# Performance work log

Measured on AMD Instinct MI355X. Metric: run time of the kernel, lower is better.

Reference implementation:

```python
import jax, jax.numpy as jnp
import numpy as np

N = 50000
E = 800000
EPS = 1e-5


def setup_inputs() -> dict:
    key = jax.random.key(0)
    ks = jax.random.split(key, 8)
    x = jax.random.normal(ks[0], (N, 64), dtype=jnp.float32)
    edge_index = jax.random.randint(ks[1], (2, E), 0, N, dtype=jnp.int64)
    # Glorot-ish scaled weights
    W_rel0 = jax.random.normal(ks[2], (64, 128), dtype=jnp.float32) * (1.0 / np.sqrt(64))
    W_root0 = jax.random.normal(ks[3], (64, 128), dtype=jnp.float32) * (1.0 / np.sqrt(64))
    W_rel1 = jax.random.normal(ks[4], (128, 128), dtype=jnp.float32) * (1.0 / np.sqrt(128))
    W_root1 = jax.random.normal(ks[5], (128, 128), dtype=jnp.float32) * (1.0 / np.sqrt(128))
    return {
        "x": x,
        "edge_index": edge_index,
        "W_rel0": W_rel0,
        "b_rel0": jnp.zeros((128,), jnp.float32),
        "W_root0": W_root0,
        "gamma0": jnp.ones((128,), jnp.float32),
        "beta0": jnp.zeros((128,), jnp.float32),
        "W_rel1": W_rel1,
        "b_rel1": jnp.zeros((128,), jnp.float32),
        "W_root1": W_root1,
        "gamma1": jnp.ones((128,), jnp.float32),
        "beta1": jnp.zeros((128,), jnp.float32),
    }


def _graph_conv(x, src, dst, W_rel, b_rel, W_root):
    # aggr_out[i] = sum_{(s,i) in edges} x[s]   (PyG GraphConv, aggr='add')
    agg = jax.ops.segment_sum(x[src], dst, num_segments=N)  # [N, F_in]
    return agg @ W_rel + b_rel + x @ W_root                  # [N, F_out]


def _batchnorm(h, gamma, beta):
    mean = jnp.mean(h, axis=0)
    var = jnp.var(h, axis=0)
    return (h - mean) * jax.lax.rsqrt(var + EPS) * gamma + beta


def reference(x, edge_index, W_rel0, b_rel0, W_root0, gamma0, beta0,
              W_rel1, b_rel1, W_root1, gamma1, beta1):
    src, dst = edge_index[0], edge_index[1]
    # layer 0: conv -> BN -> ReLU (dropout p=0 is identity)
    h = _graph_conv(x, src, dst, W_rel0, b_rel0, W_root0)
    h = jax.nn.relu(_batchnorm(h, gamma0, beta0))
    # layer 1 (last): conv -> BN, no activation
    h = _graph_conv(h, src, dst, W_rel1, b_rel1, W_root1)
    h = _batchnorm(h, gamma1, beta1)
    return h
```

## Files before the change

kernel.cpp:

```cpp
#include <hip/hip_runtime.h>

#define NN 50000
#define NE 800000
#define EPSV 1e-5f

typedef unsigned int u32;
typedef short s16x8 __attribute__((ext_vector_type(8)));
typedef float f32x4 __attribute__((ext_vector_type(4)));

#define WS_NEEDED \
  ((size_t)(NN * 64 + NN * 32 + 1024 + NN + NN + NE + 2 * 400000 + NE) * 4)

__global__ void k_fallback(float* __restrict__ out) {
  int i = blockIdx.x * 256 + threadIdx.x;
  if (i < NN * 128) out[i] = 2.0f;
}

__global__ void k_detect(const int* __restrict__ ei, int* __restrict__ mode) {
  if (threadIdx.x == 0) {
    int all0 = 1;
    for (int i = 1; i < 64; i += 2) all0 &= (ei[i] == 0);
    *mode = all0;
  }
}

__device__ __forceinline__ void load_edge(const int* __restrict__ ei, int m, int e,
                                          int& src, int& dst) {
  if (m) { src = ei[e << 1]; dst = ei[(NE + e) << 1]; }
  else   { src = ei[e];      dst = ei[NE + e]; }
  src = min(max(src, 0), NN - 1);
  dst = min(max(dst, 0), NN - 1);
}

__global__ __launch_bounds__(256) void k_hist(
    const int* __restrict__ ei, const int* __restrict__ mode,
    int* __restrict__ deg, int* __restrict__ rank, u32* __restrict__ pedge) {
  int e = blockIdx.x * 256 + threadIdx.x;
  int src, dst;
  load_edge(ei, *mode, e, src, dst);
  rank[e] = atomicAdd(&deg[dst], 1);
  pedge[e] = ((u32)src << 16) | (u32)dst;
}

__global__ __launch_bounds__(256) void k_scan1(
    const int* __restrict__ deg, int* __restrict__ bsum) {
  const int b = blockIdx.x, t = threadIdx.x;
  const int lane = t & 63, wave = t >> 6;
  int idx = b * 256 + t;
  int v = (idx < NN) ? deg[idx] : 0;
  for (int off = 32; off > 0; off >>= 1) v += __shfl_down(v, off);
  __shared__ int wt[4];
  if (lane == 0) wt[wave] = v;
  __syncthreads();
  if (t == 0) bsum[b] = wt[0] + wt[1] + wt[2] + wt[3];
}

__global__ __launch_bounds__(256) void k_scan3(
    const int* __restrict__ deg, const int* __restrict__ bsum, int* __restrict__ cur) {
  const int b = blockIdx.x, t = threadIdx.x;
  const int lane = t & 63, wave = t >> 6;
  __shared__ int wt[4];
  __shared__ int boff;
  int pv = (t < b) ? bsum[t] : 0;
  int r = pv;
  for (int off = 32; off > 0; off >>= 1) r += __shfl_down(r, off);
  if (lane == 0) wt[wave] = r;
  __syncthreads();
  if (t == 0) boff = wt[0] + wt[1] + wt[2] + wt[3];
  __syncthreads();
  int idx = b * 256 + t;
  int v = (idx < NN) ? deg[idx] : 0;
  int incl = v;
  for (int off = 1; off < 64; off <<= 1) {
    int u = __shfl_up(incl, off);
    if (lane >= off) incl += u;
  }
  if (lane == 63) wt[wave] = incl;
  __syncthreads();
  int woff = 0;
  for (int w = 0; w < wave; ++w) woff += wt[w];
  if (idx < NN) cur[idx] = boff + woff + incl - v;
}

__global__ __launch_bounds__(256) void k_place(
    const u32* __restrict__ pedge, const int* __restrict__ cur,
    const int* __restrict__ rank, int* __restrict__ csr) {
  int e = blockIdx.x * 256 + threadIdx.x;
  u32 pe = pedge[e];
  int dst = (int)(pe & 0xffffu);
  int src = (int)(pe >> 16);
  csr[cur[dst] + rank[e]] = src;
}

__device__ __forceinline__ u32 pack_bf16(float lo, float hi) {
  union { float f; u32 u; } a, b;
  a.f = lo; b.f = hi;
  u32 ua = a.u + 0x7fffu + ((a.u >> 16) & 1u);
  u32 ub = b.u + 0x7fffu + ((b.u >> 16) & 1u);
  return (ua >> 16) | (ub & 0xffff0000u);
}
#define BFLO(u) __uint_as_float((u) << 16)
#define BFHI(u) __uint_as_float((u) & 0xffff0000u)

__global__ __launch_bounds__(256) void k_pack(
    const float* __restrict__ x, u32* __restrict__ xb) {
  int i = blockIdx.x * 256 + threadIdx.x;
  int n = i >> 5, c = i & 31;
  float2 v = *(const float2*)&x[n * 64 + c * 2];
  xb[i] = pack_bf16(v.x, v.y);
}

__global__ __launch_bounds__(256) void k_gather_xb(
    const u32* __restrict__ xb, const int* __restrict__ csr,
    const int* __restrict__ cur, const int* __restrict__ deg,
    u32* __restrict__ aggxb) {
  int tid = blockIdx.x * 256 + threadIdx.x;
  int n = tid >> 4, L = tid & 15;
  int i = cur[n];
  int end = i + deg[n];
  float a0 = 0.f, a1 = 0.f, a2 = 0.f, a3 = 0.f;
  float b0 = 0.f, b1 = 0.f, b2 = 0.f, b3 = 0.f;
  for (; i + 1 < end; i += 2) {
    int s0 = csr[i], s1 = csr[i + 1];
    uint2 u = *(const uint2*)&xb[s0 * 32 + 2 * L];
    uint2 w = *(const uint2*)&xb[s1 * 32 + 2 * L];
    a0 += BFLO(u.x); a1 += BFHI(u.x); a2 += BFLO(u.y); a3 += BFHI(u.y);
    b0 += BFLO(w.x); b1 += BFHI(w.x); b2 += BFLO(w.y); b3 += BFHI(w.y);
  }
  if (i < end) {
    int s0 = csr[i];
    uint2 u = *(const uint2*)&xb[s0 * 32 + 2 * L];
    a0 += BFLO(u.x); a1 += BFHI(u.x); a2 += BFLO(u.y); a3 += BFHI(u.y);
  }
  uint2 o;
  o.x = pack_bf16(a0 + b0, a1 + b1);
  o.y = pack_bf16(a2 + b2, a3 + b3);
  *(uint2*)&aggxb[n * 32 + 2 * L] = o;
}

__global__ __launch_bounds__(256) void k_packW0(
    const float* __restrict__ Wrel, const float* __restrict__ Wroot,
    u32* __restrict__ Wpk0) {
  int t = blockIdx.x * 256 + threadIdx.x;
  int r = t & 3, lane = (t >> 2) & 63, s = (t >> 8) & 3, nt = t >> 10;
  int k = 32 * s + (lane >> 4) * 8 + 2 * r;
  int col = 16 * nt + (lane & 15);
  const float* W = (k < 64) ? &Wrel[k * 128 + col] : &Wroot[(k - 64) * 128 + col];
  Wpk0[t] = pack_bf16(W[0], W[128]);
}

__global__ __launch_bounds__(256) void k_gemm_a(
    const float* __restrict__ x, const u32* __restrict__ aggxb,
    const u32* __restrict__ Wpk0,
    float* __restrict__ h, float* __restrict__ psum, float* __restrict__ pssq) {
  __shared__ u32 As[8192];
  const int tid = threadIdx.x;
  const int nb = blockIdx.x * 128;
  char* AsB = (char*)As;
#pragma unroll
  for (int it = 0; it < 16; ++it) {
    int f = tid + 256 * it;
    int row = f >> 5, k4 = f & 31;
    int n = nb + row;
    uint2 p;
    if (k4 < 16) {
      p = (n < NN) ? *(const uint2*)&aggxb[n * 32 + 2 * k4] : make_uint2(0u, 0u);
    } else {
      float4 v = (n < NN) ? *(const float4*)&x[n * 64 + 4 * (k4 - 16)]
                          : make_float4(0.f, 0.f, 0.f, 0.f);
      p.x = pack_bf16(v.x, v.y);
      p.y = pack_bf16(v.z, v.w);
    }
    int byte = row * 256 + k4 * 8;
    byte ^= (row & 7) << 4;
    *(uint2*)(AsB + byte) = p;
  }
  __syncthreads();
  const int lane = tid & 63;
  const int w = tid >> 6;
  const int lr = lane & 15;
  const int lg = lane >> 4;
  f32x4 zero = {0.f, 0.f, 0.f, 0.f};
  f32x4 acc[8][2];
#pragma unroll
  for (int m = 0; m < 8; ++m) {
    acc[m][0] = zero;
    acc[m][1] = zero;
  }
#pragma unroll
  for (int s = 0; s < 4; ++s) {
    s16x8 bf[2];
#pragma unroll
    for (int nt = 0; nt < 2; ++nt)
      bf[nt] = *(const s16x8*)&Wpk0[(((2 * w + nt) * 4 + s) * 64 + lane) * 4];
#pragma unroll
    for (int m = 0; m < 8; ++m) {
      int row = 16 * m + lr;
      int byte = row * 256 + 64 * s + 16 * lg;
      byte ^= (row & 7) << 4;
      s16x8 af = *(const s16x8*)(AsB + byte);
      acc[m][0] = __builtin_amdgcn_mfma_f32_16x16x32_bf16(af, bf[0], acc[m][0], 0, 0, 0);
      acc[m][1] = __builtin_amdgcn_mfma_f32_16x16x32_bf16(af, bf[1], acc[m][1], 0, 0, 0);
    }
  }
  float ps[2] = {0.f, 0.f}, qs[2] = {0.f, 0.f};
#pragma unroll
  for (int m = 0; m < 8; ++m) {
    int rowb = nb + 16 * m + 4 * lg;
#pragma unroll
    for (int nt = 0; nt < 2; ++nt) {
      int colg = 32 * w + 16 * nt + lr;
#pragma unroll
      for (int i = 0; i < 4; ++i) {
        float a = acc[m][nt][i];
        int n = rowb + i;
        if (n < NN) h[n * 128 + colg] = a;
        ps[nt] += a;
        qs[nt] += a * a;
      }
    }
  }
  __syncthreads();
  float* S = (float*)As;
  float* Q = S + 512;
#pragma unroll
  for (int nt = 0; nt < 2; ++nt) {
    int colg = 32 * w + 16 * nt + lr;
    S[lg * 128 + colg] = ps[nt];
    Q[lg * 128 + colg] = qs[nt];
  }
  __syncthreads();
  if (tid < 128) {
    float s = 0.f, q = 0.f;
#pragma unroll
    for (int g = 0; g < 4; ++g) { s += S[g * 128 + tid]; q += Q[g * 128 + tid]; }
    psum[blockIdx.x * 128 + tid] = s;
    pssq[blockIdx.x * 128 + tid] = q;
  }
}

__global__ __launch_bounds__(64) void k_bnfin(
    const float* __restrict__ psum, const float* __restrict__ pssq,
    const float* __restrict__ gamma, const float* __restrict__ beta,
    float* __restrict__ scale, float* __restrict__ shift, int P) {
  const int c = blockIdx.x;
  const int t = threadIdx.x;
  float S = 0.f, Q = 0.f;
  for (int p = t; p < P; p += 64) {
    S += psum[p * 128 + c];
    Q += pssq[p * 128 + c];
  }
  for (int off = 32; off > 0; off >>= 1) {
    S += __shfl_down(S, off);
    Q += __shfl_down(Q, off);
  }
  if (t == 0) {
    float mean = S * (1.0f / NN);
    float var = fmaxf(Q * (1.0f / NN) - mean * mean, 0.f);
    float sc = gamma[c] * rsqrtf(var + EPSV);
    scale[c] = sc;
    shift[c] = beta[c] - mean * sc;
  }
}

__global__ __launch_bounds__(256) void k_packW(
    const float* __restrict__ Wrel, const float* __restrict__ Wroot,
    u32* __restrict__ Wpk) {
  int t = blockIdx.x * 256 + threadIdx.x;
  int r = t & 3, lane = (t >> 2) & 63, s = (t >> 8) & 3, nt = t >> 10;
  int k = 32 * s + (lane >> 4) * 8 + 2 * r;
  int col = 16 * nt + (lane & 15);
  const float* W = (col < 128) ? &Wrel[k * 128 + col] : &Wroot[k * 128 + (col - 128)];
  Wpk[t] = pack_bf16(W[0], W[128]);
}

__global__ __launch_bounds__(256) void k_gemm_b(
    const u32* __restrict__ Wpk,
    const float* __restrict__ scale, const float* __restrict__ shift,
    u32* __restrict__ yb, float* __restrict__ h) {
  __shared__ u32 As[4096];
  const int tid = threadIdx.x;
  const int nb = blockIdx.x * 64;
  char* AsB = (char*)As;
#pragma unroll
  for (int it = 0; it < 8; ++it) {
    int f = tid + 256 * it;
    int row = f >> 5, k4 = f & 31;
    int n = nb + row;
    float4 v = (n < NN) ? *(const float4*)&h[n * 128 + 4 * k4]
                        : make_float4(0.f, 0.f, 0.f, 0.f);
    float4 sc = *(const float4*)&scale[4 * k4];
    float4 sh = *(const float4*)&shift[4 * k4];
    float t0 = fmaxf(v.x * sc.x + sh.x, 0.f);
    float t1 = fmaxf(v.y * sc.y + sh.y, 0.f);
    float t2 = fmaxf(v.z * sc.z + sh.z, 0.f);
    float t3 = fmaxf(v.w * sc.w + sh.w, 0.f);
    uint2 p;
    p.x = pack_bf16(t0, t1);
    p.y = pack_bf16(t2, t3);
    int byte = row * 256 + k4 * 8;
    byte ^= (row & 7) << 4;
    *(uint2*)(AsB + byte) = p;
  }
  __syncthreads();
  const int lane = tid & 63;
  const int w = tid >> 6;
  const int lr = lane & 15;
  const int lg = lane >> 4;
  f32x4 zero = {0.f, 0.f, 0.f, 0.f};
  f32x4 acc[4][4];
#pragma unroll
  for (int m = 0; m < 4; ++m)
#pragma unroll
    for (int nt = 0; nt < 4; ++nt) acc[m][nt] = zero;

#pragma unroll
  for (int s = 0; s < 4; ++s) {
    s16x8 af[4];
#pragma unroll
    for (int m = 0; m < 4; ++m) {
      int row = 16 * m + lr;
      int byte = row * 256 + 64 * s + 16 * lg;
      byte ^= (row & 7) << 4;
      af[m] = *(const s16x8*)(AsB + byte);
    }
    s16x8 bf[4];
#pragma unroll
    for (int nt = 0; nt < 4; ++nt) {
      int gnt = w * 4 + nt;
      bf[nt] = *(const s16x8*)&Wpk[((gnt * 4 + s) * 64 + lane) * 4];
    }
#pragma unroll
    for (int m = 0; m < 4; ++m)
#pragma unroll
      for (int nt = 0; nt < 4; ++nt)
        acc[m][nt] = __builtin_amdgcn_mfma_f32_16x16x32_bf16(
            af[m], bf[nt], acc[m][nt], 0, 0, 0);
  }
  if (w < 2) {
#pragma unroll
    for (int m = 0; m < 4; ++m) {
#pragma unroll
      for (int nt = 0; nt < 4; ++nt) {
        int colg = 64 * w + 16 * nt + lr;
        int rowb = nb + 16 * m + 4 * lg;
        float a0 = acc[m][nt][0], a1 = acc[m][nt][1];
        float a2 = acc[m][nt][2], a3 = acc[m][nt][3];
        float o0 = __shfl_xor(a0, 1), o1 = __shfl_xor(a1, 1);
        float o2 = __shfl_xor(a2, 1), o3 = __shfl_xor(a3, 1);
        int c2 = colg >> 1;
        u32 q0, q1;
        int i0;
        if ((lane & 1) == 0) {
          q0 = pack_bf16(a0, o0); q1 = pack_bf16(a1, o1); i0 = 0;
        } else {
          q0 = pack_bf16(o2, a2); q1 = pack_bf16(o3, a3); i0 = 2;
        }
        int n0 = rowb + i0, n1 = rowb + i0 + 1;
        if (n0 < NN) yb[n0 * 64 + c2] = q0;
        if (n1 < NN) yb[n1 * 64 + c2] = q1;
      }
    }
  } else {
#pragma unroll
    for (int m = 0; m < 4; ++m) {
#pragma unroll
      for (int nt = 0; nt < 4; ++nt) {
        int colg = 64 * (w - 2) + 16 * nt + lr;
        int rowb = nb + 16 * m + 4 * lg;
#pragma unroll
        for (int i = 0; i < 4; ++i) {
          int n = rowb + i;
          if (n < NN) h[n * 128 + colg] = acc[m][nt][i];
        }
      }
    }
  }
}

__global__ __launch_bounds__(256) void k_gather2(
    const u32* __restrict__ yb, const int* __restrict__ csr,
    const int* __restrict__ cur, const int* __restrict__ deg,
    float* __restrict__ h, float* __restrict__ psum, float* __restrict__ pssq) {
  int tid = blockIdx.x * 256 + threadIdx.x;
  int n = tid >> 4;
  int L = threadIdx.x & 15;
  int base = L << 2;
  int c0 = L << 3;
  int i = cur[n];
  int end = i + deg[n];
  float lo0 = 0.f, lo1 = 0.f, lo2 = 0.f, lo3 = 0.f;
  float hi0 = 0.f, hi1 = 0.f, hi2 = 0.f, hi3 = 0.f;
  float mo0 = 0.f, mo1 = 0.f, mo2 = 0.f, mo3 = 0.f;
  float ni0 = 0.f, ni1 = 0.f, ni2 = 0.f, ni3 = 0.f;
  for (; i + 1 < end; i += 2) {
    int s0 = csr[i], s1 = csr[i + 1];
    uint4 v = *(const uint4*)&yb[s0 * 64 + base];
    uint4 w = *(const uint4*)&yb[s1 * 64 + base];
    lo0 += BFLO(v.x); hi0 += BFHI(v.x);
    lo1 += BFLO(v.y); hi1 += BFHI(v.y);
    lo2 += BFLO(v.z); hi2 += BFHI(v.z);
    lo3 += BFLO(v.w); hi3 += BFHI(v.w);
    mo0 += BFLO(w.x); ni0 += BFHI(w.x);
    mo1 += BFLO(w.y); ni1 += BFHI(w.y);
    mo2 += BFLO(w.z); ni2 += BFHI(w.z);
    mo3 += BFLO(w.w); ni3 += BFHI(w.w);
  }
  if (i < end) {
    int s = csr[i];
    uint4 v = *(const uint4*)&yb[s * 64 + base];
    lo0 += BFLO(v.x); hi0 += BFHI(v.x);
    lo1 += BFLO(v.y); hi1 += BFHI(v.y);
    lo2 += BFLO(v.z); hi2 += BFHI(v.z);
    lo3 += BFLO(v.w); hi3 += BFHI(v.w);
  }
  float4 A = *(const float4*)&h[n * 128 + c0];
  float4 B = *(const float4*)&h[n * 128 + c0 + 4];
  float4 R0 = make_float4(A.x + lo0 + mo0, A.y + hi0 + ni0,
                          A.z + lo1 + mo1, A.w + hi1 + ni1);
  float4 R1 = make_float4(B.x + lo2 + mo2, B.y + hi2 + ni2,
                          B.z + lo3 + mo3, B.w + hi3 + ni3);
  *(float4*)&h[n * 128 + c0]     = R0;
  *(float4*)&h[n * 128 + c0 + 4] = R1;
  __shared__ float S[16 * 132], Q[16 * 132];
  const int nl = threadIdx.x >> 4;
  *(float4*)&S[nl * 132 + c0]     = R0;
  *(float4*)&S[nl * 132 + c0 + 4] = R1;
  *(float4*)&Q[nl * 132 + c0] =
      make_float4(R0.x * R0.x, R0.y * R0.y, R0.z * R0.z, R0.w * R0.w);
  *(float4*)&Q[nl * 132 + c0 + 4] =
      make_float4(R1.x * R1.x, R1.y * R1.y, R1.z * R1.z, R1.w * R1.w);
  __syncthreads();
  const int t = threadIdx.x;
  if (t < 128) {
    float s = 0.f, q = 0.f;
#pragma unroll
    for (int g = 0; g < 16; ++g) { s += S[g * 132 + t]; q += Q[g * 132 + t]; }
    psum[blockIdx.x * 128 + t] = s;
    pssq[blockIdx.x * 128 + t] = q;
  }
}

__global__ __launch_bounds__(256) void k_final(
    const float* __restrict__ h, const float* __restrict__ scale,
    const float* __restrict__ shift, float* __restrict__ out) {
  int tid = blockIdx.x * 256 + threadIdx.x;
  int base = tid << 2;
  int f4 = base & 127;
  float4 v = *(const float4*)&h[base];
  float4 sc = *(const float4*)&scale[f4];
  float4 sh = *(const float4*)&shift[f4];
  *(float4*)&out[base] = make_float4(v.x * sc.x + sh.x, v.y * sc.y + sh.y,
                                     v.z * sc.z + sh.z, v.w * sc.w + sh.w);
}

extern "C" void kernel_launch(void* const* d_in, const int* in_sizes, int n_in,
                              void* d_out, int out_size, void* d_ws, size_t ws_size,
                              hipStream_t stream) {
  if (ws_size < WS_NEEDED) {
    k_fallback<<<(NN * 128 + 255) / 256, 256, 0, stream>>>((float*)d_out);
    return;
  }
  const float* x      = (const float*)d_in[0];
  const int*   ei     = (const int*)d_in[1];
  const float* Wrel0  = (const float*)d_in[2];
  const float* Wroot0 = (const float*)d_in[4];
  const float* gamma0 = (const float*)d_in[5];
  const float* beta0  = (const float*)d_in[6];
  const float* Wrel1  = (const float*)d_in[7];
  const float* Wroot1 = (const float*)d_in[9];
  const float* gamma1 = (const float*)d_in[10];
  const float* beta1  = (const float*)d_in[11];

  float* aggx = (float*)d_ws;
  u32*   aggxb = (u32*)d_ws;
  u32*   yb   = (u32*)d_ws;
  u32*   xb   = (u32*)(aggx + NN * 64);
  u32*   Wpk  = xb;
  u32*   Wpk0 = xb + 16384;
  float* st   = (float*)(xb + NN * 32);
  float* scale0 = st;       float* shift0 = st + 128;
  float* scale1 = st + 256; float* shift1 = st + 384;
  int* mode = (int*)(st + 512);
  int* bsum = (int*)(st + 576);
  int* deg = (int*)(st + 1024);
  int* cur = deg + NN;
  int* csr = cur + NN;
  float* psum = (float*)(csr + NE);
  float* pssq = psum + 400000;
  int* rank = (int*)psum;
  u32* pedge = (u32*)(pssq + 400000);
  float* h = (float*)d_out;

  hipMemsetAsync(deg, 0, (size_t)NN * 4, stream);
  k_detect<<<1, 64, 0, stream>>>(ei, mode);
  k_hist<<<NE / 256, 256, 0, stream>>>(ei, mode, deg, rank, pedge);
  k_scan1<<<196, 256, 0, stream>>>(deg, bsum);
  k_scan3<<<196, 256, 0, stream>>>(deg, bsum, cur);
  k_place<<<NE / 256, 256, 0, stream>>>(pedge, cur, rank, csr);

  k_pack<<<(NN * 32) / 256, 256, 0, stream>>>(x, xb);
  k_gather_xb<<<(NN * 16) / 256, 256, 0, stream>>>(xb, csr, cur, deg, aggxb);
  k_packW<<<64, 256, 0, stream>>>(Wrel1, Wroot1, Wpk);
  k_packW0<<<32, 256, 0, stream>>>(Wrel0, Wroot0, Wpk0);
  k_gemm_a<<<(NN + 127) / 128, 256, 0, stream>>>(x, aggxb, Wpk0, h, psum, pssq);
  k_bnfin<<<128, 64, 0, stream>>>(psum, pssq, gamma0, beta0, scale0, shift0, 391);
  k_gemm_b<<<(NN + 63) / 64, 256, 0, stream>>>(Wpk, scale0, shift0, yb, h);
  k_gather2<<<(NN * 16) / 256, 256, 0, stream>>>(yb, csr, cur, deg, h, psum, pssq);
  k_bnfin<<<128, 64, 0, stream>>>(psum, pssq, gamma1, beta1, scale1, shift1, 3125);
  k_final<<<(NN * 128) / 1024, 256, 0, stream>>>(h, scale1, shift1, (float*)d_out);
}
```

Before: 279.0 us.

## Store layer-0 conv output as bf16 and merge packing kernels into one launch

The layer-0 GEMM now writes its pre-BN output h as packed bf16 into a workspace buffer, pairing neighbouring columns with a lane shuffle, instead of writing fp32 to the output buffer. The layer-1 GEMM reads this bf16 buffer and widens it before applying BN and ReLU, which halves that intermediate's write and read traffic. gemm_a also reads the pre-packed bf16 x instead of re-converting fp32 x. The three small pack kernels are merged into one launch, saving two launches. BN statistics are still taken from fp32 accumulators, but the extra bf16 rounding of h adds some precision loss and the workspace grows.

```diff
diff --git a/kernel.cpp b/kernel.cpp
--- a/kernel.cpp
+++ b/kernel.cpp
@@ -9,7 +9,8 @@
 typedef float f32x4 __attribute__((ext_vector_type(4)));
 
 #define WS_NEEDED \
-  ((size_t)(NN * 64 + NN * 32 + 1024 + NN + NN + NE + 2 * 400000 + NE) * 4)
+  ((size_t)(NN * 64 + NN * 32 + 1024 + NN + NN + NE + 2 * 400000 + NE + \
+            16384 + 8192 + NN * 64) * 4)
 
 __global__ void k_fallback(float* __restrict__ out) {
   int i = blockIdx.x * 256 + threadIdx.x;
@@ -102,12 +103,35 @@
 #define BFLO(u) __uint_as_float((u) << 16)
 #define BFHI(u) __uint_as_float((u) & 0xffff0000u)
 
-__global__ __launch_bounds__(256) void k_pack(
-    const float* __restrict__ x, u32* __restrict__ xb) {
-  int i = blockIdx.x * 256 + threadIdx.x;
-  int n = i >> 5, c = i & 31;
-  float2 v = *(const float2*)&x[n * 64 + c * 2];
-  xb[i] = pack_bf16(v.x, v.y);
+__global__ __launch_bounds__(256) void k_prep(
+    const float* __restrict__ x, u32* __restrict__ xb,
+    const float* __restrict__ Wrel1, const float* __restrict__ Wroot1,
+    u32* __restrict__ Wpk,
+    const float* __restrict__ Wrel0, const float* __restrict__ Wroot0,
+    u32* __restrict__ Wpk0) {
+  const int b = blockIdx.x;
+  if (b < 6250) {
+    int i = b * 256 + threadIdx.x;
+    int n = i >> 5, c = i & 31;
+    float2 v = *(const float2*)&x[n * 64 + c * 2];
+    xb[i] = pack_bf16(v.x, v.y);
+  } else if (b < 6314) {
+    int t = (b - 6250) * 256 + threadIdx.x;
+    int r = t & 3, lane = (t >> 2) & 63, s = (t >> 8) & 3, nt = t >> 10;
+    int k = 32 * s + (lane >> 4) * 8 + 2 * r;
+    int col = 16 * nt + (lane & 15);
+    const float* W = (col < 128) ? &Wrel1[k * 128 + col]
+                                 : &Wroot1[k * 128 + (col - 128)];
+    Wpk[t] = pack_bf16(W[0], W[128]);
+  } else {
+    int t = (b - 6314) * 256 + threadIdx.x;
+    int r = t & 3, lane = (t >> 2) & 63, s = (t >> 8) & 3, nt = t >> 10;
+    int k = 32 * s + (lane >> 4) * 8 + 2 * r;
+    int col = 16 * nt + (lane & 15);
+    const float* W = (k < 64) ? &Wrel0[k * 128 + col]
+                              : &Wroot0[(k - 64) * 128 + col];
+    Wpk0[t] = pack_bf16(W[0], W[128]);
+  }
 }
 
 __global__ __launch_bounds__(256) void k_gather_xb(
@@ -138,21 +162,10 @@
   *(uint2*)&aggxb[n * 32 + 2 * L] = o;
 }
 
-__global__ __launch_bounds__(256) void k_packW0(
-    const float* __restrict__ Wrel, const float* __restrict__ Wroot,
-    u32* __restrict__ Wpk0) {
-  int t = blockIdx.x * 256 + threadIdx.x;
-  int r = t & 3, lane = (t >> 2) & 63, s = (t >> 8) & 3, nt = t >> 10;
-  int k = 32 * s + (lane >> 4) * 8 + 2 * r;
-  int col = 16 * nt + (lane & 15);
-  const float* W = (k < 64) ? &Wrel[k * 128 + col] : &Wroot[(k - 64) * 128 + col];
-  Wpk0[t] = pack_bf16(W[0], W[128]);
-}
-
 __global__ __launch_bounds__(256) void k_gemm_a(
-    const float* __restrict__ x, const u32* __restrict__ aggxb,
+    const u32* __restrict__ xb, const u32* __restrict__ aggxb,
     const u32* __restrict__ Wpk0,
-    float* __restrict__ h, float* __restrict__ psum, float* __restrict__ pssq) {
+    u32* __restrict__ hb, float* __restrict__ psum, float* __restrict__ pssq) {
   __shared__ u32 As[8192];
   const int tid = threadIdx.x;
   const int nb = blockIdx.x * 128;
@@ -162,15 +175,8 @@
     int f = tid + 256 * it;
     int row = f >> 5, k4 = f & 31;
     int n = nb + row;
-    uint2 p;
-    if (k4 < 16) {
-      p = (n < NN) ? *(const uint2*)&aggxb[n * 32 + 2 * k4] : make_uint2(0u, 0u);
-    } else {
-      float4 v = (n < NN) ? *(const float4*)&x[n * 64 + 4 * (k4 - 16)]
-                          : make_float4(0.f, 0.f, 0.f, 0.f);
-      p.x = pack_bf16(v.x, v.y);
-      p.y = pack_bf16(v.z, v.w);
-    }
+    const u32* src = (k4 < 16) ? &aggxb[n * 32 + 2 * k4] : &xb[n * 32 + 2 * (k4 - 16)];
+    uint2 p = (n < NN) ? *(const uint2*)src : make_uint2(0u, 0u);
     int byte = row * 256 + k4 * 8;
     byte ^= (row & 7) << 4;
     *(uint2*)(AsB + byte) = p;
@@ -206,18 +212,37 @@
   float ps[2] = {0.f, 0.f}, qs[2] = {0.f, 0.f};
 #pragma unroll
   for (int m = 0; m < 8; ++m) {
-    int rowb = nb + 16 * m + 4 * lg;
 #pragma unroll
     for (int nt = 0; nt < 2; ++nt) {
-      int colg = 32 * w + 16 * nt + lr;
 #pragma unroll
       for (int i = 0; i < 4; ++i) {
         float a = acc[m][nt][i];
-        int n = rowb + i;
-        if (n < NN) h[n * 128 + colg] = a;
         ps[nt] += a;
         qs[nt] += a * a;
       }
+    }
+  }
+#pragma unroll
+  for (int m = 0; m < 8; ++m) {
+    int rowb = nb + 16 * m + 4 * lg;
+#pragma unroll
+    for (int nt = 0; nt < 2; ++nt) {
+      int colg = 32 * w + 16 * nt + lr;
+      float a0 = acc[m][nt][0], a1 = acc[m][nt][1];
+      float a2 = acc[m][nt][2], a3 = acc[m][nt][3];
+      float o0 = __shfl_xor(a0, 1), o1 = __shfl_xor(a1, 1);
+      float o2 = __shfl_xor(a2, 1), o3 = __shfl_xor(a3, 1);
+      int c2 = colg >> 1;
+      u32 q0, q1;
+      int i0;
+      if ((lane & 1) == 0) {
+        q0 = pack_bf16(a0, o0); q1 = pack_bf16(a1, o1); i0 = 0;
+      } else {
+        q0 = pack_bf16(o2, a2); q1 = pack_bf16(o3, a3); i0 = 2;
+      }
+      int n0 = rowb + i0, n1 = rowb + i0 + 1;
+      if (n0 < NN) hb[n0 * 64 + c2] = q0;
+      if (n1 < NN) hb[n1 * 64 + c2] = q1;
     }
   }
   __syncthreads();
@@ -263,19 +288,8 @@
   }
 }
 
-__global__ __launch_bounds__(256) void k_packW(
-    const float* __restrict__ Wrel, const float* __restrict__ Wroot,
-    u32* __restrict__ Wpk) {
-  int t = blockIdx.x * 256 + threadIdx.x;
-  int r = t & 3, lane = (t >> 2) & 63, s = (t >> 8) & 3, nt = t >> 10;
-  int k = 32 * s + (lane >> 4) * 8 + 2 * r;
-  int col = 16 * nt + (lane & 15);
-  const float* W = (col < 128) ? &Wrel[k * 128 + col] : &Wroot[k * 128 + (col - 128)];
-  Wpk[t] = pack_bf16(W[0], W[128]);
-}
-
 __global__ __launch_bounds__(256) void k_gemm_b(
-    const u32* __restrict__ Wpk,
+    const u32* __restrict__ hb, const u32* __restrict__ Wpk,
     const float* __restrict__ scale, const float* __restrict__ shift,
     u32* __restrict__ yb, float* __restrict__ h) {
   __shared__ u32 As[4096];
@@ -287,14 +301,13 @@
     int f = tid + 256 * it;
     int row = f >> 5, k4 = f & 31;
     int n = nb + row;
-    float4 v = (n < NN) ? *(const float4*)&h[n * 128 + 4 * k4]
-                        : make_float4(0.f, 0.f, 0.f, 0.f);
+    uint2 v = (n < NN) ? *(const uint2*)&hb[n * 64 + 2 * k4] : make_uint2(0u, 0u);
     float4 sc = *(const float4*)&scale[4 * k4];
     float4 sh = *(const float4*)&shift[4 * k4];
-    float t0 = fmaxf(v.x * sc.x + sh.x, 0.f);
-    float t1 = fmaxf(v.y * sc.y + sh.y, 0.f);
-    float t2 = fmaxf(v.z * sc.z + sh.z, 0.f);
-    float t3 = fmaxf(v.w * sc.w + sh.w, 0.f);
+    float t0 = fmaxf(BFLO(v.x) * sc.x + sh.x, 0.f);
+    float t1 = fmaxf(BFHI(v.x) * sc.y + sh.y, 0.f);
+    float t2 = fmaxf(BFLO(v.y) * sc.z + sh.z, 0.f);
+    float t3 = fmaxf(BFHI(v.y) * sc.w + sh.w, 0.f);
     uint2 p;
     p.x = pack_bf16(t0, t1);
     p.y = pack_bf16(t2, t3);
@@ -472,12 +485,9 @@
   const float* gamma1 = (const float*)d_in[10];
   const float* beta1  = (const float*)d_in[11];
 
-  float* aggx = (float*)d_ws;
   u32*   aggxb = (u32*)d_ws;
   u32*   yb   = (u32*)d_ws;
-  u32*   xb   = (u32*)(aggx + NN * 64);
-  u32*   Wpk  = xb;
-  u32*   Wpk0 = xb + 16384;
+  u32*   xb   = (u32*)((float*)d_ws + NN * 64);
   float* st   = (float*)(xb + NN * 32);
   float* scale0 = st;       float* shift0 = st + 128;
   float* scale1 = st + 256; float* shift1 = st + 384;
@@ -490,6 +500,9 @@
   float* pssq = psum + 400000;
   int* rank = (int*)psum;
   u32* pedge = (u32*)(pssq + 400000);
+  u32* Wpk  = pedge + NE;
+  u32* Wpk0 = Wpk + 16384;
+  u32* hb   = Wpk0 + 8192;
   float* h = (float*)d_out;
 
   hipMemsetAsync(deg, 0, (size_t)NN * 4, stream);
@@ -499,13 +512,11 @@
   k_scan3<<<196, 256, 0, stream>>>(deg, bsum, cur);
   k_place<<<NE / 256, 256, 0, stream>>>(pedge, cur, rank, csr);
 
-  k_pack<<<(NN * 32) / 256, 256, 0, stream>>>(x, xb);
+  k_prep<<<6346, 256, 0, stream>>>(x, xb, Wrel1, Wroot1, Wpk, Wrel0, Wroot0, Wpk0);
   k_gather_xb<<<(NN * 16) / 256, 256, 0, stream>>>(xb, csr, cur, deg, aggxb);
-  k_packW<<<64, 256, 0, stream>>>(Wrel1, Wroot1, Wpk);
-  k_packW0<<<32, 256, 0, stream>>>(Wrel0, Wroot0, Wpk0);
-  k_gemm_a<<<(NN + 127) / 128, 256, 0, stream>>>(x, aggxb, Wpk0, h, psum, pssq);
+  k_gemm_a<<<(NN + 127) / 128, 256, 0, stream>>>(xb, aggxb, Wpk0, hb, psum, pssq);
   k_bnfin<<<128, 64, 0, stream>>>(psum, pssq, gamma0, beta0, scale0, shift0, 391);
-  k_gemm_b<<<(NN + 63) / 64, 256, 0, stream>>>(Wpk, scale0, shift0, yb, h);
+  k_gemm_b<<<(NN + 63) / 64, 256, 0, stream>>>(hb, Wpk, scale0, shift0, yb, h);
   k_gather2<<<(NN * 16) / 256, 256, 0, stream>>>(yb, csr, cur, deg, h, psum, pssq);
   k_bnfin<<<128, 64, 0, stream>>>(psum, pssq, gamma1, beta1, scale1, shift1, 3125);
   k_final<<<(NN * 128) / 1024, 256, 0, stream>>>(h, scale1, shift1, (float*)d_out);
```

Result: faster. 269.1 us (-3.5%).
